# Kernel tuning notes

Hardware: AMD Instinct MI355X
Metric: run time of the kernel (lower is better)

## Reference

```python
import jax, jax.numpy as jnp
import numpy as np

DIM = 1024
NUM_HEADS = 16
HEAD_DIM = DIM // NUM_HEADS
SCALE = HEAD_DIM ** -0.5


def setup_inputs() -> dict:
    key = jax.random.key(0)
    ks = jax.random.split(key, 5)
    x = jax.random.normal(ks[0], (8, 1024, DIM), dtype=jnp.float32)
    # nn.Linear default init ~ U(-1/sqrt(fan_in), 1/sqrt(fan_in)); use scaled normals
    w_qkv = jax.random.normal(ks[1], (DIM, 3 * DIM), dtype=jnp.float32) * (DIM ** -0.5)
    b_qkv = jax.random.normal(ks[2], (3 * DIM,), dtype=jnp.float32) * 0.02
    w_proj = jax.random.normal(ks[3], (DIM, DIM), dtype=jnp.float32) * (DIM ** -0.5)
    b_proj = jax.random.normal(ks[4], (DIM,), dtype=jnp.float32) * 0.02
    return {"x": x, "w_qkv": w_qkv, "b_qkv": b_qkv, "w_proj": w_proj, "b_proj": b_proj}


def reference(x, w_qkv, b_qkv, w_proj, b_proj):
    B, N, D = x.shape
    qkv = x @ w_qkv + b_qkv                       # [B, N, 3D]
    qkv = qkv.reshape(B, N, 3, NUM_HEADS, HEAD_DIM)
    qkv = jnp.transpose(qkv, (2, 0, 3, 1, 4))     # [3, B, H, N, hd]
    q, k, v = qkv[0], qkv[1], qkv[2]
    attn = jnp.einsum('bhqd,bhkd->bhqk', q, k) * SCALE
    attn = jax.nn.softmax(attn, axis=-1)
    out = jnp.einsum('bhqk,bhkd->bhqd', attn, v)  # [B, H, N, hd]
    out = jnp.transpose(out, (0, 2, 1, 3)).reshape(B, N, D)
    out = out @ w_proj + b_proj
    return out
```

## Files before the change

### kernel.cpp

```cpp
#include <hip/hip_runtime.h>
#include <stdint.h>


typedef short bf16x8 __attribute__((ext_vector_type(8)));
typedef float f32x4 __attribute__((ext_vector_type(4)));
typedef uint32_t u32x2 __attribute__((ext_vector_type(2)));

__device__ __forceinline__ short f32_bf16(float f) {
  uint32_t u = __builtin_bit_cast(uint32_t, f);
  u += 0x7FFFu + ((u >> 16) & 1u);
  return (short)(u >> 16);
}

__device__ __forceinline__ float exp2_fast(float x) {
  float r; asm("v_exp_f32 %0, %1" : "=v"(r) : "v"(x)); return r;
}

__device__ __forceinline__ uint32_t cvt_pk_bf16(float lo, float hi) {
  uint32_t r;
  asm("v_cvt_pk_bf16_f32 %0, %1, %2" : "=v"(r) : "v"(lo), "v"(hi));
  return r;
}

__device__ __forceinline__ void gload_lds16(const void* g, void* l) {
  __builtin_amdgcn_global_load_lds(
      (const __attribute__((address_space(1))) uint32_t*)g,
      (__attribute__((address_space(3))) uint32_t*)l, 16, 0, 0);
}

__global__ __launch_bounds__(256) void convert_x_kernel(
    const float* __restrict__ x, short* __restrict__ xb) {
  int i = blockIdx.x * 256 + threadIdx.x;
  const float4 f0 = ((const float4*)x)[i * 2];
  const float4 f1 = ((const float4*)x)[i * 2 + 1];
  bf16x8 o;
  o[0] = f32_bf16(f0.x); o[1] = f32_bf16(f0.y);
  o[2] = f32_bf16(f0.z); o[3] = f32_bf16(f0.w);
  o[4] = f32_bf16(f1.x); o[5] = f32_bf16(f1.y);
  o[6] = f32_bf16(f1.z); o[7] = f32_bf16(f1.w);
  ((bf16x8*)xb)[i] = o;
}

__global__ __launch_bounds__(256) void transpose_w_kernel(
    const float* __restrict__ w, short* __restrict__ wt, int N) {
  __shared__ float tile[64][65];
  const int n0 = blockIdx.x * 64, k0 = blockIdx.y * 64;
  const int tr = threadIdx.x >> 6, tc = threadIdx.x & 63;
#pragma unroll
  for (int i = 0; i < 16; ++i) {
    int k = tr + i * 4;
    tile[k][tc] = w[(size_t)(k0 + k) * N + n0 + tc];
  }
  __syncthreads();
#pragma unroll
  for (int i = 0; i < 16; ++i) {
    int a = tr + i * 4;
    wt[(size_t)(n0 + a) * 1024 + k0 + tc] = f32_bf16(tile[tc][a]);
  }
}

template <int BN, int NREP, int BCH, int EPI>
__global__ __launch_bounds__(512, 2) void gemm8_kernel(
    const short* __restrict__ A, const short* __restrict__ Bt,
    const float* __restrict__ bias, short* __restrict__ Qb,
    short* __restrict__ Kb, short* __restrict__ Vt, float* __restrict__ out,
    int NTN) {
  __shared__ short Asm[2][256 * 64];
  __shared__ short Bsm[2][BN * 64];

  constexpr int TOT = 4 + BCH;
  constexpr int CS2 = (TOT == 8) ? 6 : 5;
  constexpr int NPP = NREP / 2;
  constexpr int WN = NREP * 16;

  const int tid = threadIdx.x;
  const int lane = tid & 63;
  const int w = tid >> 6;
  const int wm = w >> 2, wn = w & 3;
  const int c = lane & 15, g = lane >> 4;

  const int nwg = gridDim.x;
  const int wg = (blockIdx.x & 7) * (nwg >> 3) + (blockIdx.x >> 3);
  const int tm = wg / NTN, tn = wg % NTN;
  const int m0 = tm * 256, n0 = tn * BN;

  f32x4 acc[8][NREP] = {};

  auto stage_chunk = [&](int ci, int dbuf, int kk0) {
    if (ci < 4) {
      const int p = ci * 512 + tid;
      const int r = p >> 3, s = p & 7;
      gload_lds16(A + (size_t)(m0 + r) * 1024 + kk0 + ((s ^ (r & 7)) * 8),
                  &Asm[dbuf][p * 8]);
    } else {
      const int p = (ci - 4) * 512 + tid;
      const int r = p >> 3, s = p & 7;
      gload_lds16(Bt + (size_t)(n0 + r) * 1024 + kk0 + ((s ^ (r & 7)) * 8),
                  &Bsm[dbuf][p * 8]);
    }
  };

#pragma unroll
  for (int ci = 0; ci < TOT; ++ci) stage_chunk(ci, 0, 0);

  auto tile_step = [&](int t, int buf) {
#pragma unroll
    for (int p4 = 0; p4 < 4; ++p4) {
      const int cs = (p4 == 0) ? 0 : (p4 == 1) ? 2 : (p4 == 2) ? 4 : CS2;
      const int ce = (p4 == 0) ? 2 : (p4 == 1) ? 4 : (p4 == 2) ? CS2 : TOT;
      if (t < 15) {
#pragma unroll
        for (int ci = cs; ci < ce; ++ci) stage_chunk(ci, buf ^ 1, (t + 1) * 64);
      }
      if (p4 == 0) {
        if (t < 15) asm volatile("s_waitcnt vmcnt(2)" ::: "memory");
        else        asm volatile("s_waitcnt vmcnt(0)" ::: "memory");
        __builtin_amdgcn_s_barrier();
      }
      const int mq = p4 >> 1, nq = p4 & 1;
      bf16x8 af[4][2];
      bf16x8 bfr[NPP][2];
#pragma unroll
      for (int mm = 0; mm < 4; ++mm) {
        const int R = wm * 128 + (mq * 4 + mm) * 16 + c;
#pragma unroll
        for (int kk = 0; kk < 2; ++kk)
          af[mm][kk] = *(const bf16x8*)&Asm[buf][R * 64 + (((kk * 4 + g) ^ (c & 7)) * 8)];
      }
#pragma unroll
      for (int jn = 0; jn < NPP; ++jn) {
        const int S = wn * WN + (nq * NPP + jn) * 16 + c;
#pragma unroll
        for (int kk = 0; kk < 2; ++kk)
          bfr[jn][kk] = *(const bf16x8*)&Bsm[buf][S * 64 + (((kk * 4 + g) ^ (c & 7)) * 8)];
      }
      __builtin_amdgcn_s_barrier();
      asm volatile("s_waitcnt lgkmcnt(0)" ::: "memory");
      __builtin_amdgcn_sched_barrier(0);
      __builtin_amdgcn_s_setprio(1);
#pragma unroll
      for (int mm = 0; mm < 4; ++mm)
#pragma unroll
        for (int jn = 0; jn < NPP; ++jn)
#pragma unroll
          for (int kk = 0; kk < 2; ++kk)
            acc[mq * 4 + mm][nq * NPP + jn] = __builtin_amdgcn_mfma_f32_16x16x32_bf16(
                af[mm][kk], bfr[jn][kk], acc[mq * 4 + mm][nq * NPP + jn], 0, 0, 0);
      __builtin_amdgcn_s_setprio(0);
      __builtin_amdgcn_s_barrier();
    }
  };

  for (int t2 = 0; t2 < 16; t2 += 2) {
    tile_step(t2, 0);
    tile_step(t2 + 1, 1);
  }

#pragma unroll
  for (int mm = 0; mm < 8; ++mm) {
    const int i_base = m0 + wm * 128 + mm * 16 + 4 * g;
#pragma unroll
    for (int nn = 0; nn < NREP; ++nn) {
      const int j = n0 + wn * WN + nn * 16 + c;
      const float bj = bias[j];
      if (EPI == 0) {
        const int three = j >> 10, rem = j & 1023, h = rem >> 6, d = rem & 63;
        const float sc = (three == 1) ? 0.18033688f : 1.0f;
#pragma unroll
        for (int r = 0; r < 4; ++r) {
          const int i = i_base + r;
          const int bb = i >> 10, nnq = i & 1023;
          const int bh = bb * 16 + h;
          const short bv = f32_bf16((acc[mm][nn][r] + bj) * sc);
          if (three == 0)
            Qb[(size_t)(bh * 1024 + nnq) * 64 + d] = bv;
          else if (three == 1)
            Kb[(size_t)(bh * 1024 + nnq) * 64 + d] = bv;
          else
            Vt[(size_t)(bh * 64 + d) * 1024 + nnq] = bv;
        }
      } else {
#pragma unroll
        for (int r = 0; r < 4; ++r)
          out[(size_t)(i_base + r) * 1024 + j] = acc[mm][nn][r] + bj;
      }
    }
  }
}

__global__ __launch_bounds__(256, 2) void attn_kernel(
    const short* __restrict__ Qb, const short* __restrict__ Kb,
    const short* __restrict__ Vt, short* __restrict__ Ao) {
  __shared__ __align__(16) char smem[25600];
  short* Kf = (short*)smem;
  short* Vf = (short*)(smem + 8192);
  short* Pl = (short*)(smem + 16384);

  const int tid = threadIdx.x, lane = tid & 63, w = tid >> 6;
  const int c = lane & 15, g = lane >> 4;
  const int bh = blockIdx.x >> 3, qb = blockIdx.x & 7;
  const int bb = bh >> 4, h = bh & 15;
  const int q0 = qb * 128 + w * 32;

  bf16x8 qf[2][2];
#pragma unroll
  for (int m = 0; m < 2; ++m)
#pragma unroll
    for (int ks = 0; ks < 2; ++ks)
      qf[m][ks] = *(const bf16x8*)(Qb + (size_t)(bh * 1024 + q0 + m * 16 + c) * 64 + ks * 32 + 8 * g);

  f32x4 o[2][4] = {};
  float mrun[2] = {-3.0e38f, -3.0e38f};
  float lrun[2] = {0.f, 0.f};

  const int row_r = tid >> 2, seg = tid & 3;
  const short* kp = Kb + (size_t)(bh * 1024 + row_r) * 64 + seg * 16;
  const short* vp = Vt + (size_t)(bh * 64 + row_r) * 1024 + seg * 16;
  short *kdst0, *kdst1, *vdst0, *vdst1;
  {
    const int d0a = seg * 16, d0b = seg * 16 + 8;
    const int pa = (row_r >> 4) * 2 + (d0a >> 5);
    const int pb = (row_r >> 4) * 2 + (d0b >> 5);
    const int sa = (row_r & 15) + 16 * ((d0a & 31) >> 3);
    const int sb = (row_r & 15) + 16 * ((d0b & 31) >> 3);
    kdst0 = &Kf[(pa * 64 + sa) * 8]; kdst1 = &Kf[(pb * 64 + sb) * 8];
    vdst0 = &Vf[(pa * 64 + sa) * 8]; vdst1 = &Vf[(pb * 64 + sb) * 8];
  }

  uint32_t* plw = (uint32_t*)(Pl + w * 1152);
  const short* plr = Pl + w * 1152;

  auto compute = [&]() {
#pragma unroll
    for (int m = 0; m < 2; ++m) {
      f32x4 s[4];
#pragma unroll
      for (int kt = 0; kt < 4; ++kt) {
        f32x4 sa = {};
#pragma unroll
        for (int ks = 0; ks < 2; ++ks) {
          bf16x8 kb = *(const bf16x8*)&Kf[((kt * 2 + ks) * 64 + lane) * 8];
          sa = __builtin_amdgcn_mfma_f32_16x16x32_bf16(kb, qf[m][ks], sa, 0, 0, 0);
        }
        s[kt] = sa;
      }
      float vmax = s[0][0];
#pragma unroll
      for (int kt = 0; kt < 4; ++kt)
#pragma unroll
        for (int r = 0; r < 4; ++r) vmax = fmaxf(vmax, s[kt][r]);
      vmax = fmaxf(vmax, __shfl_xor(vmax, 16));
      vmax = fmaxf(vmax, __shfl_xor(vmax, 32));
      if (!__all(vmax <= mrun[m] + 8.0f)) {
        float mnew = fmaxf(mrun[m], vmax);
        float al = exp2_fast(mrun[m] - mnew);
        lrun[m] *= al;
#pragma unroll
        for (int dt = 0; dt < 4; ++dt) o[m][dt] *= al;
        mrun[m] = mnew;
      }
      float rs = 0.f;
#pragma unroll
      for (int kt = 0; kt < 4; ++kt) {
        float p0 = exp2_fast(s[kt][0] - mrun[m]);
        float p1 = exp2_fast(s[kt][1] - mrun[m]);
        float p2 = exp2_fast(s[kt][2] - mrun[m]);
        float p3 = exp2_fast(s[kt][3] - mrun[m]);
        rs += (p0 + p1) + (p2 + p3);
        u32x2 pk;
        pk[0] = cvt_pk_bf16(p0, p1);
        pk[1] = cvt_pk_bf16(p2, p3);
        *(u32x2*)&plw[c * 36 + kt * 8 + 2 * g] = pk;
      }
      rs += __shfl_xor(rs, 16);
      rs += __shfl_xor(rs, 32);
      lrun[m] += rs;
#pragma unroll
      for (int kk = 0; kk < 2; ++kk) {
        bf16x8 pb = *(const bf16x8*)(plr + c * 72 + kk * 32 + 8 * g);
#pragma unroll
        for (int dt = 0; dt < 4; ++dt) {
          bf16x8 vb = *(const bf16x8*)&Vf[((dt * 2 + kk) * 64 + lane) * 8];
          o[m][dt] = __builtin_amdgcn_mfma_f32_16x16x32_bf16(vb, pb, o[m][dt], 0, 0, 0);
        }
      }
    }
  };

  bf16x8 ka0, ka1, va0, va1, kc0, kc1, vc0, vc1;
  ka0 = *(const bf16x8*)(kp);     ka1 = *(const bf16x8*)(kp + 8);
  va0 = *(const bf16x8*)(vp);     va1 = *(const bf16x8*)(vp + 8);

  for (int t = 0; t < 16; t += 2) {
    __syncthreads();
    *(bf16x8*)kdst0 = ka0; *(bf16x8*)kdst1 = ka1;
    *(bf16x8*)vdst0 = va0; *(bf16x8*)vdst1 = va1;
    {
      const short* kpt = kp + (size_t)(t + 1) * 4096;
      const short* vpt = vp + (t + 1) * 64;
      kc0 = *(const bf16x8*)(kpt); kc1 = *(const bf16x8*)(kpt + 8);
      vc0 = *(const bf16x8*)(vpt); vc1 = *(const bf16x8*)(vpt + 8);
    }
    __syncthreads();
    compute();
    __syncthreads();
    *(bf16x8*)kdst0 = kc0; *(bf16x8*)kdst1 = kc1;
    *(bf16x8*)vdst0 = vc0; *(bf16x8*)vdst1 = vc1;
    if (t + 2 < 16) {
      const short* kpt = kp + (size_t)(t + 2) * 4096;
      const short* vpt = vp + (t + 2) * 64;
      ka0 = *(const bf16x8*)(kpt); ka1 = *(const bf16x8*)(kpt + 8);
      va0 = *(const bf16x8*)(vpt); va1 = *(const bf16x8*)(vpt + 8);
    }
    __syncthreads();
    compute();
  }

  __syncthreads();
  float* Osc = (float*)smem + w * (16 * 68);
  const int qrow = lane >> 2, dseg = (lane & 3) << 4;
#pragma unroll
  for (int m = 0; m < 2; ++m) {
    const float inv = 1.0f / lrun[m];
#pragma unroll
    for (int dt = 0; dt < 4; ++dt)
#pragma unroll
      for (int r = 0; r < 4; ++r)
        Osc[c * 68 + dt * 16 + 4 * g + r] = o[m][dt][r] * inv;
#pragma unroll
    for (int j = 0; j < 2; ++j) {
      f32x4 a0 = *(f32x4*)&Osc[qrow * 68 + dseg + j * 8];
      f32x4 a1 = *(f32x4*)&Osc[qrow * 68 + dseg + j * 8 + 4];
      bf16x8 ob;
      ob[0] = f32_bf16(a0[0]); ob[1] = f32_bf16(a0[1]);
      ob[2] = f32_bf16(a0[2]); ob[3] = f32_bf16(a0[3]);
      ob[4] = f32_bf16(a1[0]); ob[5] = f32_bf16(a1[1]);
      ob[6] = f32_bf16(a1[2]); ob[7] = f32_bf16(a1[3]);
      *(bf16x8*)(Ao + (size_t)(bb * 1024 + q0 + m * 16 + qrow) * 1024 + h * 64 + dseg + j * 8) = ob;
    }
    __syncthreads();
  }
}

extern "C" void kernel_launch(void* const* d_in, const int* in_sizes, int n_in,
                              void* d_out, int out_size, void* d_ws, size_t ws_size,
                              hipStream_t stream) {
  const float* x = (const float*)d_in[0];
  const float* w_qkv = (const float*)d_in[1];
  const float* b_qkv = (const float*)d_in[2];
  const float* w_proj = (const float*)d_in[3];
  const float* b_proj = (const float*)d_in[4];
  float* out = (float*)d_out;

  char* ws = (char*)d_ws;
  const size_t XB_OFF = 0;
  const size_t WQKVT_OFF = 16777216;
  const size_t WPROJT_OFF = WQKVT_OFF + 6291456;
  const size_t Q_OFF = WPROJT_OFF + 2097152;
  const size_t K_OFF = Q_OFF + 16777216;
  const size_t VT_OFF = K_OFF + 16777216;
  short* xb = (short*)(ws + XB_OFF);
  short* wqkvT = (short*)(ws + WQKVT_OFF);
  short* wprojT = (short*)(ws + WPROJT_OFF);
  short* Qb = (short*)(ws + Q_OFF);
  short* Kb = (short*)(ws + K_OFF);
  short* Vt = (short*)(ws + VT_OFF);
  short* attn_o = xb;

  convert_x_kernel<<<dim3(4096), dim3(256), 0, stream>>>(x, xb);
  transpose_w_kernel<<<dim3(48, 16), dim3(256), 0, stream>>>(w_qkv, wqkvT, 3072);
  transpose_w_kernel<<<dim3(16, 16), dim3(256), 0, stream>>>(w_proj, wprojT, 1024);
  gemm8_kernel<256, 4, 4, 0><<<dim3(384), dim3(512), 0, stream>>>(
      xb, wqkvT, b_qkv, Qb, Kb, Vt, nullptr, 12);
  attn_kernel<<<dim3(1024), dim3(256), 0, stream>>>(Qb, Kb, Vt, attn_o);
  gemm8_kernel<128, 2, 2, 1><<<dim3(256), dim3(512), 0, stream>>>(
      attn_o, wprojT, b_proj, nullptr, nullptr, nullptr, out, 8);
}
```

Before: 311.7 us.

## Simplify GEMM pipeline to one barrier pair per K-step and shrink QKV tile

Replaces the four-phase interleaved load/compute schedule, which staged chunks across sub-steps with extra barriers, with a simpler loop. Each K-step now issues all next-tile loads up front, waits, then computes two M-halves while reusing B fragments. The QKV GEMM switches from 256x256 to 256x128 tiles, doubling the grid to 768 blocks, and launch bounds drop to one block per CU. The aim is fewer barriers and better load balance, at the cost of less B reuse, more A traffic and possibly lower occupancy.

```diff
diff --git a/kernel.cpp b/kernel.cpp
--- a/kernel.cpp
+++ b/kernel.cpp
@@ -59,19 +59,14 @@
   }
 }
 
-template <int BN, int NREP, int BCH, int EPI>
-__global__ __launch_bounds__(512, 2) void gemm8_kernel(
+template <int EPI>
+__global__ __launch_bounds__(512, 1) void gemm8_kernel(
     const short* __restrict__ A, const short* __restrict__ Bt,
     const float* __restrict__ bias, short* __restrict__ Qb,
     short* __restrict__ Kb, short* __restrict__ Vt, float* __restrict__ out,
     int NTN) {
   __shared__ short Asm[2][256 * 64];
-  __shared__ short Bsm[2][BN * 64];
-
-  constexpr int TOT = 4 + BCH;
-  constexpr int CS2 = (TOT == 8) ? 6 : 5;
-  constexpr int NPP = NREP / 2;
-  constexpr int WN = NREP * 16;
+  __shared__ short Bsm[2][128 * 64];
 
   const int tid = threadIdx.x;
   const int lane = tid & 63;
@@ -82,9 +77,9 @@
   const int nwg = gridDim.x;
   const int wg = (blockIdx.x & 7) * (nwg >> 3) + (blockIdx.x >> 3);
   const int tm = wg / NTN, tn = wg % NTN;
-  const int m0 = tm * 256, n0 = tn * BN;
-
-  f32x4 acc[8][NREP] = {};
+  const int m0 = tm * 256, n0 = tn * 128;
+
+  f32x4 acc[8][2] = {};
 
   auto stage_chunk = [&](int ci, int dbuf, int kk0) {
     if (ci < 4) {
@@ -101,25 +96,31 @@
   };
 
 #pragma unroll
-  for (int ci = 0; ci < TOT; ++ci) stage_chunk(ci, 0, 0);
-
-  auto tile_step = [&](int t, int buf) {
-#pragma unroll
-    for (int p4 = 0; p4 < 4; ++p4) {
-      const int cs = (p4 == 0) ? 0 : (p4 == 1) ? 2 : (p4 == 2) ? 4 : CS2;
-      const int ce = (p4 == 0) ? 2 : (p4 == 1) ? 4 : (p4 == 2) ? CS2 : TOT;
-      if (t < 15) {
-#pragma unroll
-        for (int ci = cs; ci < ce; ++ci) stage_chunk(ci, buf ^ 1, (t + 1) * 64);
-      }
-      if (p4 == 0) {
-        if (t < 15) asm volatile("s_waitcnt vmcnt(2)" ::: "memory");
-        else        asm volatile("s_waitcnt vmcnt(0)" ::: "memory");
-        __builtin_amdgcn_s_barrier();
-      }
-      const int mq = p4 >> 1, nq = p4 & 1;
+  for (int ci = 0; ci < 6; ++ci) stage_chunk(ci, 0, 0);
+
+  for (int t = 0; t < 16; ++t) {
+    const int buf = t & 1;
+    if (t < 15) {
+#pragma unroll
+      for (int ci = 0; ci < 6; ++ci) stage_chunk(ci, buf ^ 1, (t + 1) * 64);
+      asm volatile("s_waitcnt vmcnt(6)" ::: "memory");
+    } else {
+      asm volatile("s_waitcnt vmcnt(0)" ::: "memory");
+    }
+    __builtin_amdgcn_s_barrier();
+    __builtin_amdgcn_sched_barrier(0);
+
+    bf16x8 bfr[2][2];
+#pragma unroll
+    for (int jn = 0; jn < 2; ++jn) {
+      const int S = wn * 32 + jn * 16 + c;
+#pragma unroll
+      for (int kk = 0; kk < 2; ++kk)
+        bfr[jn][kk] = *(const bf16x8*)&Bsm[buf][S * 64 + (((kk * 4 + g) ^ (c & 7)) * 8)];
+    }
+#pragma unroll
+    for (int mq = 0; mq < 2; ++mq) {
       bf16x8 af[4][2];
-      bf16x8 bfr[NPP][2];
 #pragma unroll
       for (int mm = 0; mm < 4; ++mm) {
         const int R = wm * 128 + (mq * 4 + mm) * 16 + c;
@@ -127,41 +128,29 @@
         for (int kk = 0; kk < 2; ++kk)
           af[mm][kk] = *(const bf16x8*)&Asm[buf][R * 64 + (((kk * 4 + g) ^ (c & 7)) * 8)];
       }
-#pragma unroll
-      for (int jn = 0; jn < NPP; ++jn) {
-        const int S = wn * WN + (nq * NPP + jn) * 16 + c;
-#pragma unroll
-        for (int kk = 0; kk < 2; ++kk)
-          bfr[jn][kk] = *(const bf16x8*)&Bsm[buf][S * 64 + (((kk * 4 + g) ^ (c & 7)) * 8)];
-      }
-      __builtin_amdgcn_s_barrier();
       asm volatile("s_waitcnt lgkmcnt(0)" ::: "memory");
       __builtin_amdgcn_sched_barrier(0);
       __builtin_amdgcn_s_setprio(1);
 #pragma unroll
       for (int mm = 0; mm < 4; ++mm)
 #pragma unroll
-        for (int jn = 0; jn < NPP; ++jn)
+        for (int jn = 0; jn < 2; ++jn)
 #pragma unroll
           for (int kk = 0; kk < 2; ++kk)
-            acc[mq * 4 + mm][nq * NPP + jn] = __builtin_amdgcn_mfma_f32_16x16x32_bf16(
-                af[mm][kk], bfr[jn][kk], acc[mq * 4 + mm][nq * NPP + jn], 0, 0, 0);
+            acc[mq * 4 + mm][jn] = __builtin_amdgcn_mfma_f32_16x16x32_bf16(
+                af[mm][kk], bfr[jn][kk], acc[mq * 4 + mm][jn], 0, 0, 0);
       __builtin_amdgcn_s_setprio(0);
-      __builtin_amdgcn_s_barrier();
-    }
-  };
-
-  for (int t2 = 0; t2 < 16; t2 += 2) {
-    tile_step(t2, 0);
-    tile_step(t2 + 1, 1);
+    }
+    __builtin_amdgcn_s_barrier();
+    __builtin_amdgcn_sched_barrier(0);
   }
 
 #pragma unroll
   for (int mm = 0; mm < 8; ++mm) {
     const int i_base = m0 + wm * 128 + mm * 16 + 4 * g;
 #pragma unroll
-    for (int nn = 0; nn < NREP; ++nn) {
-      const int j = n0 + wn * WN + nn * 16 + c;
+    for (int nn = 0; nn < 2; ++nn) {
+      const int j = n0 + wn * 32 + nn * 16 + c;
       const float bj = bias[j];
       if (EPI == 0) {
         const int three = j >> 10, rem = j & 1023, h = rem >> 6, d = rem & 63;
@@ -370,9 +359,9 @@
   convert_x_kernel<<<dim3(4096), dim3(256), 0, stream>>>(x, xb);
   transpose_w_kernel<<<dim3(48, 16), dim3(256), 0, stream>>>(w_qkv, wqkvT, 3072);
   transpose_w_kernel<<<dim3(16, 16), dim3(256), 0, stream>>>(w_proj, wprojT, 1024);
-  gemm8_kernel<256, 4, 4, 0><<<dim3(384), dim3(512), 0, stream>>>(
-      xb, wqkvT, b_qkv, Qb, Kb, Vt, nullptr, 12);
+  gemm8_kernel<0><<<dim3(768), dim3(512), 0, stream>>>(
+      xb, wqkvT, b_qkv, Qb, Kb, Vt, nullptr, 24);
   attn_kernel<<<dim3(1024), dim3(256), 0, stream>>>(Qb, Kb, Vt, attn_o);
-  gemm8_kernel<128, 2, 2, 1><<<dim3(256), dim3(512), 0, stream>>>(
+  gemm8_kernel<1><<<dim3(256), dim3(512), 0, stream>>>(
       attn_o, wprojT, b_proj, nullptr, nullptr, nullptr, out, 8);
 }
```

After: 284.8 us. 8.6% less time.
